# Kernel optimization log

Measured on AMD Instinct MI355X. Metric: run time of the kernel, lower is better.

The kernel has to match this reference:

```python
import jax, jax.numpy as jnp
import numpy as np

N_NODES = 50000
N_EDGES = 400000
N_GRAPHS = 256
HID = 128
FEAT_IN, POS_IN, EDGE_IN = 64, 16, 16
N_LAYERS = 4


def _lin(x, w, b):
    return x @ w.T + b


def setup_inputs() -> dict:
    key = jax.random.key(0)
    ks = iter(jax.random.split(key, 64))
    s = 0.05

    def w(shape):
        return (jax.random.normal(next(ks), shape, dtype=jnp.float32) * s)

    inp = {
        "h": jax.random.normal(next(ks), (N_NODES, FEAT_IN), dtype=jnp.float32),
        "e": jax.random.normal(next(ks), (N_EDGES, EDGE_IN), dtype=jnp.float32),
        "p": jax.random.normal(next(ks), (N_NODES, POS_IN), dtype=jnp.float32),
        "edge_index": jax.random.randint(next(ks), (2, N_EDGES), 0, N_NODES),
        "batch": jnp.sort(jax.random.randint(next(ks), (N_NODES,), 0, N_GRAPHS)),
        # embeddings
        "h_embed_w": w((HID, FEAT_IN)), "h_embed_b": w((HID,)),
        "e_embed_w": w((HID, EDGE_IN)), "e_embed_b": w((HID,)),
        "p_embed_w": w((HID, POS_IN)), "p_embed_b": w((HID,)),
        # per-layer params, stacked over layers
        "hu_w": w((N_LAYERS, HID, 5 * HID)), "hu_b": w((N_LAYERS, HID)),
        "eu_w": w((N_LAYERS, HID, 3 * HID)), "eu_b": w((N_LAYERS, HID)),
        "pu_w": w((N_LAYERS, HID, 3 * HID)), "pu_b": w((N_LAYERS, HID)),
        "hagg_w": w((N_LAYERS, HID, 2 * HID)), "hagg_b": w((N_LAYERS, HID)),
        "pagg_w": w((N_LAYERS, HID, 2 * HID)), "pagg_b": w((N_LAYERS, HID)),
        # readout MLP
        "r1_w": w((HID, 2 * HID)), "r1_b": w((HID,)),
        "r2_w": w((HID // 2, HID)), "r2_b": w((HID // 2,)),
        "r3_w": w((1, HID // 2)), "r3_b": w((1,)),
    }
    return inp


def reference(h, e, p, edge_index, batch,
              h_embed_w, h_embed_b, e_embed_w, e_embed_b, p_embed_w, p_embed_b,
              hu_w, hu_b, eu_w, eu_b, pu_w, pu_b,
              hagg_w, hagg_b, pagg_w, pagg_b,
              r1_w, r1_b, r2_w, r2_b, r3_w, r3_b):
    send, rec = edge_index[0], edge_index[1]
    N = h.shape[0]

    h = _lin(h, h_embed_w, h_embed_b)
    e = _lin(e, e_embed_w, e_embed_b)
    p = _lin(p, p_embed_w, p_embed_b)

    for l in range(N_LAYERS):
        hp_send = jnp.concatenate((h[send], p[send]), axis=1)  # [E, 2H]
        hp_rec = jnp.concatenate((h[rec], p[rec]), axis=1)     # [E, 2H]
        h_msg = _lin(jnp.concatenate((hp_send, hp_rec, e), axis=1), hu_w[l], hu_b[l])
        h_msg_agg = jax.ops.segment_sum(h_msg, rec, num_segments=N)
        h = _lin(jnp.concatenate((h, h_msg_agg), axis=1), hagg_w[l], hagg_b[l])
        e = _lin(jnp.concatenate((h[send], h[rec], e), axis=1), eu_w[l], eu_b[l])
        p_msg = _lin(jnp.concatenate((p[send], p[rec], e), axis=1), pu_w[l], pu_b[l])
        p_msg_agg = jax.ops.segment_sum(p_msg, rec, num_segments=N)
        p = _lin(jnp.concatenate((p, p_msg_agg), axis=1), pagg_w[l], pagg_b[l])

    h_agg = jax.ops.segment_sum(h, batch, num_segments=N_GRAPHS)
    p_agg = jax.ops.segment_sum(p, batch, num_segments=N_GRAPHS)
    hep = jnp.concatenate((h_agg, p_agg), axis=1)
    x = jax.nn.relu(_lin(hep, r1_w, r1_b))
    x = jax.nn.relu(_lin(x, r2_w, r2_b))
    out = _lin(x, r3_w, r3_b).squeeze(-1)  # [N_GRAPHS]
    return (out, p)
```

## Files before the change

kernel.cpp:

```cpp
#include <hip/hip_runtime.h>

typedef __attribute__((ext_vector_type(8))) short bf16x8;
typedef __attribute__((ext_vector_type(4))) float f32x4;
typedef __attribute__((ext_vector_type(4))) unsigned short us4;

__device__ __forceinline__ float b2f(unsigned short h) {
  union { unsigned int u; float f; } v; v.u = ((unsigned int)h) << 16; return v.f;
}
__device__ __forceinline__ unsigned short f2b(float f) {
  union { float f; unsigned int u; } v; v.f = f;
  unsigned int r = v.u + 0x7fffu + ((v.u >> 16) & 1u);
  return (unsigned short)(r >> 16);
}

__device__ __forceinline__ bf16x8 scale8(bf16x8 a, float d) {
  bf16x8 r;
#pragma unroll
  for (int i = 0; i < 8; ++i) {
    union { unsigned int u; float f; } v;
    v.u = ((unsigned int)(unsigned short)a[i]) << 16;
    v.f *= d;
    r[i] = (short)(v.u >> 16);
  }
  return r;
}

__global__ void f2b_kernel(const float* __restrict__ in, unsigned short* __restrict__ out, int n4) {
  int i = blockIdx.x * blockDim.x + threadIdx.x;
  int stride = gridDim.x * blockDim.x;
  for (; i < n4; i += stride) {
    float4 v = reinterpret_cast<const float4*>(in)[i];
    us4 o;
    o[0] = f2b(v.x); o[1] = f2b(v.y); o[2] = f2b(v.z); o[3] = f2b(v.w);
    reinterpret_cast<us4*>(out)[i] = o;
  }
}

__launch_bounds__(256)
__global__ void compose_w(const float* __restrict__ hg, const float* __restrict__ hu,
                          const float* __restrict__ pg, const float* __restrict__ pu,
                          const float* __restrict__ hub, const float* __restrict__ pub,
                          unsigned short* __restrict__ wh, unsigned short* __restrict__ wp,
                          float* __restrict__ bh, float* __restrict__ bp) {
  __shared__ float As[128][129];
  __shared__ float Bs[128][36];
  __shared__ float bvs[128];
  const int l = blockIdx.x >> 5, t = blockIdx.x & 31;
  const float* A; const float* B; const float* bv; unsigned short* W; float* bo;
  int lda, ldb, ldw, cbase, wbase, dbase;
  if (t < 20) {
    A = hg + (size_t)l * 128 * 256; lda = 256;
    B = hu + (size_t)l * 128 * 640; ldb = 640;
    W = wh + (size_t)l * 128 * 768; ldw = 768;
    bv = hub + l * 128; bo = bh + l * 128; cbase = t * 32;
    wbase = (cbase < 256) ? cbase : (cbase < 512 ? cbase + 256 : cbase - 256);
    dbase = 384;
  } else {
    A = pg + (size_t)l * 128 * 256; lda = 256;
    B = pu + (size_t)l * 128 * 384; ldb = 384;
    W = wp + (size_t)l * 128 * 512; ldw = 512;
    bv = pub + l * 128; bo = bp + l * 128; cbase = (t - 20) * 32;
    wbase = (cbase < 128) ? cbase : (cbase < 256 ? cbase + 256 : cbase - 128);
    dbase = 256;
  }
  const int tid = threadIdx.x;
  for (int idx = tid; idx < 128 * 128; idx += 256) {
    int r = idx >> 7, c = idx & 127;
    As[r][c] = A[r * lda + 128 + c];
  }
  for (int idx = tid; idx < 128 * 32; idx += 256) {
    int m = idx >> 5, c = idx & 31;
    Bs[m][c] = B[m * ldb + cbase + c];
  }
  if (tid < 128) bvs[tid] = bv[tid];
  __syncthreads();
  const int o = tid & 127, g = tid >> 7;
  float acc[16];
#pragma unroll
  for (int j = 0; j < 16; ++j) acc[j] = 0.f;
  for (int m = 0; m < 128; ++m) {
    float a = As[o][m];
#pragma unroll
    for (int j4 = 0; j4 < 4; ++j4) {
      float4 b4 = *reinterpret_cast<const float4*>(&Bs[m][g * 16 + j4 * 4]);
      acc[j4 * 4 + 0] += a * b4.x; acc[j4 * 4 + 1] += a * b4.y;
      acc[j4 * 4 + 2] += a * b4.z; acc[j4 * 4 + 3] += a * b4.w;
    }
  }
#pragma unroll
  for (int j4 = 0; j4 < 4; ++j4) {
    us4 ov;
    ov[0] = f2b(acc[j4 * 4 + 0]); ov[1] = f2b(acc[j4 * 4 + 1]);
    ov[2] = f2b(acc[j4 * 4 + 2]); ov[3] = f2b(acc[j4 * 4 + 3]);
    *reinterpret_cast<us4*>(&W[(long)o * ldw + wbase + g * 16 + j4 * 4]) = ov;
  }
  if (cbase == 0) {
    for (int idx = tid; idx < 128 * 128; idx += 256) {
      int oo = idx >> 7, m = idx & 127;
      W[(long)oo * ldw + dbase + m] = f2b(A[oo * lda + m]);
    }
    if (tid < 128) {
      float s = 0.f;
      for (int m = 0; m < 128; ++m) s += As[tid][m] * bvs[m];
      bo[tid] = s;
    }
  }
}

template<int K>
__launch_bounds__(256)
__global__ void embed_fast(const float* __restrict__ in, const float* __restrict__ w,
                           const float* __restrict__ b, unsigned short* __restrict__ out,
                           long M, int ostride, int ocoloff, const float* __restrict__ degB) {
  __shared__ float wT[K][129];
  __shared__ float xt[16 * K];
  const int tid = threadIdx.x;
  const int col = tid & 127;
  const int half = tid >> 7;
  for (int idx = tid; idx < 128 * K; idx += 256) {
    int c = idx / K, k = idx % K;
    wT[k][c] = w[idx];
  }
  __syncthreads();
  float wreg[K];
#pragma unroll
  for (int k = 0; k < K; ++k) wreg[k] = wT[k][col];
  const float bcol = b[col];

  for (long r0 = (long)blockIdx.x * 16; r0 < M; r0 += (long)gridDim.x * 16) {
    __syncthreads();
    const float4* src4 = reinterpret_cast<const float4*>(in + r0 * K);
    const int n4 = 16 * K / 4;
    if (r0 + 16 <= M) {
      for (int i = tid; i < n4; i += 256)
        reinterpret_cast<float4*>(xt)[i] = src4[i];
    } else {
      int rem = (int)((M - r0) * K) / 4;
      for (int i = tid; i < n4; i += 256) {
        float4 z = {0.f, 0.f, 0.f, 0.f};
        reinterpret_cast<float4*>(xt)[i] = (i < rem) ? src4[i] : z;
      }
    }
    __syncthreads();
#pragma unroll
    for (int rr = 0; rr < 8; ++rr) {
      long row = r0 + half * 8 + rr;
      if (row >= M) break;
      const float* xr = &xt[(half * 8 + rr) * K];
      float acc = bcol * (degB ? degB[row] : 1.0f);
#pragma unroll
      for (int k4 = 0; k4 < K / 4; ++k4) {
        float4 xv = reinterpret_cast<const float4*>(xr)[k4];
        acc += xv.x * wreg[k4 * 4] + xv.y * wreg[k4 * 4 + 1] +
               xv.z * wreg[k4 * 4 + 2] + xv.w * wreg[k4 * 4 + 3];
      }
      out[row * ostride + ocoloff + col] = f2b(acc);
    }
  }
}

__global__ void count_deg(const int* __restrict__ rec, int* __restrict__ deg, int E) {
  int i = blockIdx.x * blockDim.x + threadIdx.x;
  if (i < E) atomicAdd(&deg[rec[i]], 1);
}

__global__ void scan_blk(const int* __restrict__ deg, int* __restrict__ tmp,
                         int* __restrict__ blkSum, int N) {
  __shared__ int ts[256];
  const int b = blockIdx.x, t = threadIdx.x;
  const int base = b * 1024 + t * 4;
  int v0 = (base + 0 < N) ? deg[base + 0] : 0;
  int v1 = (base + 1 < N) ? deg[base + 1] : 0;
  int v2 = (base + 2 < N) ? deg[base + 2] : 0;
  int v3 = (base + 3 < N) ? deg[base + 3] : 0;
  int tsum = v0 + v1 + v2 + v3;
  ts[t] = tsum;
  __syncthreads();
  for (int off = 1; off < 256; off <<= 1) {
    int x = (t >= off) ? ts[t - off] : 0;
    __syncthreads();
    ts[t] += x;
    __syncthreads();
  }
  int texcl = ts[t] - tsum;
  if (base + 0 < N) tmp[base + 0] = texcl;
  if (base + 1 < N) tmp[base + 1] = texcl + v0;
  if (base + 2 < N) tmp[base + 2] = texcl + v0 + v1;
  if (base + 3 < N) tmp[base + 3] = texcl + v0 + v1 + v2;
  if (t == 255) blkSum[b] = ts[255];
}

__global__ void scan_top(int* __restrict__ blkSum, int nb) {
  __shared__ int s[64];
  int t = threadIdx.x;
  if (t < nb) s[t] = blkSum[t];
  __syncthreads();
  if (t == 0) {
    int run = 0;
    for (int i = 0; i < nb; ++i) { int x = s[i]; s[i] = run; run += x; }
  }
  __syncthreads();
  if (t < nb) blkSum[t] = s[t];
}

__global__ void scan_fix(const int* __restrict__ deg, int* __restrict__ row_ptr,
                         const int* __restrict__ blkOff, int* __restrict__ cursor,
                         float* __restrict__ degF, int N, int E) {
  const int b = blockIdx.x, t = threadIdx.x;
  const int base = b * 1024 + t * 4;
  const int off = blkOff[b];
#pragma unroll
  for (int k = 0; k < 4; ++k) {
    int i = base + k;
    if (i < N) {
      int v = row_ptr[i] + off;
      row_ptr[i] = v;
      cursor[i] = v;
      degF[i] = (float)deg[i];
    }
  }
  if (b == 0 && t == 0) row_ptr[N] = E;
}

__global__ void scatter_perm(const int* __restrict__ rec, const int* __restrict__ send,
                             int* __restrict__ cursor, int* __restrict__ perm,
                             int* __restrict__ sendP, int E) {
  int i = blockIdx.x * blockDim.x + threadIdx.x;
  if (i < E) {
    int pos = atomicAdd(&cursor[rec[i]], 1);
    perm[pos] = i;
    sendP[pos] = send[i];
  }
}

__global__ void segsum_raw(const float* __restrict__ eraw, const int* __restrict__ row_ptr,
                           const int* __restrict__ perm, float* __restrict__ out16, int N) {
  int sub = threadIdx.x >> 4;
  int f = threadIdx.x & 15;
  int r = blockIdx.x * 16 + sub;
  if (r >= N) return;
  int j0 = row_ptr[r], j1 = row_ptr[r + 1];
  float s0 = 0.f, s1 = 0.f;
  int j = j0;
  for (; j + 2 <= j1; j += 2) {
    int e0 = perm[j], e1 = perm[j + 1];
    s0 += eraw[(long)e0 * 16 + f];
    s1 += eraw[(long)e1 * 16 + f];
  }
  if (j < j1) s0 += eraw[(long)perm[j] * 16 + f];
  out16[(long)r * 16 + f] = s0 + s1;
}

__launch_bounds__(256)
__global__ void gather_sum256(const unsigned short* __restrict__ src,
                              const int* __restrict__ row_ptr, const int* __restrict__ sendP,
                              unsigned short* __restrict__ dst, int N) {
  const int wid = threadIdx.x >> 6, lane = threadIdx.x & 63;
  const int r = blockIdx.x * 4 + wid;
  if (r >= N) return;
  const int j0 = row_ptr[r], j1 = row_ptr[r + 1];
  const int off = lane * 4;
  float a0 = 0.f, a1 = 0.f, a2 = 0.f, a3 = 0.f;
  int j = j0;
  for (; j + 4 <= j1; j += 4) {
    int i0 = sendP[j], i1 = sendP[j + 1], i2 = sendP[j + 2], i3 = sendP[j + 3];
    us4 x = *reinterpret_cast<const us4*>(&src[(long)i0 * 256 + off]);
    us4 y = *reinterpret_cast<const us4*>(&src[(long)i1 * 256 + off]);
    us4 z = *reinterpret_cast<const us4*>(&src[(long)i2 * 256 + off]);
    us4 w = *reinterpret_cast<const us4*>(&src[(long)i3 * 256 + off]);
    a0 += b2f(x[0]) + b2f(y[0]) + b2f(z[0]) + b2f(w[0]);
    a1 += b2f(x[1]) + b2f(y[1]) + b2f(z[1]) + b2f(w[1]);
    a2 += b2f(x[2]) + b2f(y[2]) + b2f(z[2]) + b2f(w[2]);
    a3 += b2f(x[3]) + b2f(y[3]) + b2f(z[3]) + b2f(w[3]);
  }
  for (; j < j1; ++j) {
    us4 x = *reinterpret_cast<const us4*>(&src[(long)sendP[j] * 256 + off]);
    a0 += b2f(x[0]); a1 += b2f(x[1]); a2 += b2f(x[2]); a3 += b2f(x[3]);
  }
  us4 o;
  o[0] = f2b(a0); o[1] = f2b(a1); o[2] = f2b(a2); o[3] = f2b(a3);
  *reinterpret_cast<us4*>(&dst[(long)r * 256 + off]) = o;
}

__launch_bounds__(256)
__global__ void gather_sum128(const unsigned short* __restrict__ src, int col,
                              const int* __restrict__ row_ptr, const int* __restrict__ sendP,
                              unsigned short* __restrict__ dst, int N) {
  const int wid = threadIdx.x >> 6, lane = threadIdx.x & 63;
  const int r = blockIdx.x * 4 + wid;
  if (r >= N) return;
  const int j0 = row_ptr[r], j1 = row_ptr[r + 1];
  const int half = lane >> 5;
  const int c = lane & 31;
  const int off = col + c * 4;
  float a0 = 0.f, a1 = 0.f, a2 = 0.f, a3 = 0.f;
  float b0 = 0.f, b1 = 0.f, b2 = 0.f, b3 = 0.f;
  int j = j0 + half;
  for (; j + 6 < j1; j += 8) {
    int i0 = sendP[j], i1 = sendP[j + 2], i2 = sendP[j + 4], i3 = sendP[j + 6];
    us4 x = *reinterpret_cast<const us4*>(&src[(long)i0 * 256 + off]);
    us4 y = *reinterpret_cast<const us4*>(&src[(long)i1 * 256 + off]);
    us4 z = *reinterpret_cast<const us4*>(&src[(long)i2 * 256 + off]);
    us4 w = *reinterpret_cast<const us4*>(&src[(long)i3 * 256 + off]);
    a0 += b2f(x[0]) + b2f(z[0]); a1 += b2f(x[1]) + b2f(z[1]);
    a2 += b2f(x[2]) + b2f(z[2]); a3 += b2f(x[3]) + b2f(z[3]);
    b0 += b2f(y[0]) + b2f(w[0]); b1 += b2f(y[1]) + b2f(w[1]);
    b2 += b2f(y[2]) + b2f(w[2]); b3 += b2f(y[3]) + b2f(w[3]);
  }
  for (; j + 2 < j1; j += 4) {
    int i0 = sendP[j], i1 = sendP[j + 2];
    us4 x = *reinterpret_cast<const us4*>(&src[(long)i0 * 256 + off]);
    us4 y = *reinterpret_cast<const us4*>(&src[(long)i1 * 256 + off]);
    a0 += b2f(x[0]); a1 += b2f(x[1]); a2 += b2f(x[2]); a3 += b2f(x[3]);
    b0 += b2f(y[0]); b1 += b2f(y[1]); b2 += b2f(y[2]); b3 += b2f(y[3]);
  }
  if (j < j1) {
    us4 x = *reinterpret_cast<const us4*>(&src[(long)sendP[j] * 256 + off]);
    a0 += b2f(x[0]); a1 += b2f(x[1]); a2 += b2f(x[2]); a3 += b2f(x[3]);
  }
  a0 += b0; a1 += b1; a2 += b2; a3 += b3;
  a0 += __shfl_xor(a0, 32); a1 += __shfl_xor(a1, 32);
  a2 += __shfl_xor(a2, 32); a3 += __shfl_xor(a3, 32);
  if (half == 0) {
    us4 o;
    o[0] = f2b(a0); o[1] = f2b(a1); o[2] = f2b(a2); o[3] = f2b(a3);
    *reinterpret_cast<us4*>(&dst[(long)r * 256 + off]) = o;
  }
}

__launch_bounds__(256, 3)
__global__ void gemm_mp(int M, int nsrc, int Kw, int srcsel, int coloffs, int sflags,
                        const unsigned short* __restrict__ sp0, const unsigned short* __restrict__ sp1,
                        const unsigned short* __restrict__ sp2,
                        const unsigned short* __restrict__ Wb,
                        const float* __restrict__ bdeg, const float* __restrict__ bone,
                        const float* __restrict__ degF,
                        unsigned short* __restrict__ outB, int ostride, int ocoloff,
                        float* __restrict__ outF) {
  __shared__ __align__(16) unsigned short ldsW[8 * 64 * 8];
  const int tid = threadIdx.x;
  const int wid = tid >> 6, lane = tid & 63;
  const long rowBase = (long)blockIdx.x * 128 + wid * 32;
  const int lq = lane >> 4;
  const int lr = lane & 15;

  int rowD[2];
  float degD[2];
#pragma unroll
  for (int am = 0; am < 2; ++am) {
    long e = rowBase + am * 16 + lr;
    if (e >= M) e = M - 1;
    rowD[am] = (int)e;
    degD[am] = degF[rowD[am]];
  }

  f32x4 acc[2][8];
#pragma unroll
  for (int i = 0; i < 2; ++i)
#pragma unroll
    for (int j = 0; j < 8; ++j) acc[i][j] = 0.f;

  int wcol = 0;
  for (int si = 0; si < nsrc; ++si) {
    const int sel = (srcsel >> (si * 4)) & 15;
    const unsigned short* sp = (sel == 0) ? sp0 : (sel == 1) ? sp1 : sp2;
    const long astride = (sel == 2) ? 128 : 256;
    const int acoloff = ((coloffs >> (si * 4)) & 15) * 128;
    const int f = (sflags >> (si * 4)) & 15;
    const int nrep = (f == 1) ? 2 : 1;
#pragma unroll 4
    for (int sub = 0; sub < 4; ++sub) {
      const int koff = acoloff + sub * 32 + lq * 8;
      bf16x8 a[2];
#pragma unroll
      for (int am = 0; am < 2; ++am)
        a[am] = *reinterpret_cast<const bf16x8*>(&sp[(long)rowD[am] * astride + koff]);
      for (int rep = 0; rep < nrep; ++rep) {
        const bool sc = (f == 2) || (rep == 1);
        const int wk = wcol + rep * 128 + sub * 32;
        __syncthreads();
#pragma unroll
        for (int it = 0; it < 2; ++it) {
          int idx = tid + it * 256;
          int t = idx >> 6, l = idx & 63;
          int n = t * 16 + (l & 15);
          int kk = wk + ((l >> 4) * 8);
          *reinterpret_cast<bf16x8*>(&ldsW[idx * 8]) =
              *reinterpret_cast<const bf16x8*>(&Wb[(long)n * Kw + kk]);
        }
        __syncthreads();
        bf16x8 av0 = sc ? scale8(a[0], degD[0]) : a[0];
        bf16x8 av1 = sc ? scale8(a[1], degD[1]) : a[1];
#pragma unroll
        for (int n = 0; n < 8; ++n) {
          bf16x8 b = *reinterpret_cast<const bf16x8*>(&ldsW[(n * 64 + lane) * 8]);
          acc[0][n] = __builtin_amdgcn_mfma_f32_16x16x32_bf16(av0, b, acc[0][n], 0, 0, 0);
          acc[1][n] = __builtin_amdgcn_mfma_f32_16x16x32_bf16(av1, b, acc[1][n], 0, 0, 0);
        }
      }
    }
    wcol += nrep * 128;
  }

  float bd[8], bo[8];
#pragma unroll
  for (int n = 0; n < 8; ++n) {
    bd[n] = bdeg ? bdeg[n * 16 + lr] : 0.f;
    bo[n] = bone ? bone[n * 16 + lr] : 0.f;
  }

#pragma unroll
  for (int am = 0; am < 2; ++am) {
#pragma unroll
    for (int r = 0; r < 4; ++r) {
      long row = rowBase + am * 16 + lq * 4 + r;
      if (row < M) {
        float d = degF[row];
        long ob = row * ostride + ocoloff;
#pragma unroll
        for (int n = 0; n < 8; ++n) {
          float v = acc[am][n][r] + bd[n] * d + bo[n];
          outB[ob + n * 16 + lr] = f2b(v);
          if (outF) outF[row * 128 + n * 16 + lr] = v;
        }
      }
    }
  }
}

__global__ void readout_agg(const unsigned short* __restrict__ hp,
                            const int* __restrict__ batch, float* __restrict__ hep, int N) {
  int col = threadIdx.x;
  int n0 = blockIdx.x * 128;
  int n1 = n0 + 128; if (n1 > N) n1 = N;
  float sum = 0.f; int curg = -1;
  for (int n = n0; n < n1; ++n) {
    int g = batch[n];
    if (g != curg) {
      if (curg >= 0) unsafeAtomicAdd(&hep[(long)curg * 256 + col], sum);
      curg = g; sum = 0.f;
    }
    sum += b2f(hp[(long)n * 256 + col]);
  }
  if (curg >= 0) unsafeAtomicAdd(&hep[(long)curg * 256 + col], sum);
}

__global__ void mlp_kernel(const float* __restrict__ hep,
                           const float* __restrict__ r1w, const float* __restrict__ r1b,
                           const float* __restrict__ r2w, const float* __restrict__ r2b,
                           const float* __restrict__ r3w, const float* __restrict__ r3b,
                           float* __restrict__ out) {
  int g = blockIdx.x, t = threadIdx.x;
  __shared__ float x[256];
  __shared__ float y[128];
  __shared__ float z[64];
  x[t] = hep[(long)g * 256 + t];
  x[t + 128] = hep[(long)g * 256 + 128 + t];
  __syncthreads();
  float s = r1b[t];
  for (int k = 0; k < 256; ++k) s += r1w[t * 256 + k] * x[k];
  y[t] = fmaxf(s, 0.f);
  __syncthreads();
  if (t < 64) {
    float s2 = r2b[t];
    for (int k = 0; k < 128; ++k) s2 += r2w[t * 128 + k] * y[k];
    z[t] = fmaxf(s2, 0.f);
  }
  __syncthreads();
  if (t == 0) {
    float s3 = r3b[0];
    for (int k = 0; k < 64; ++k) s3 += r3w[k] * z[k];
    out[g] = s3;
  }
}

extern "C" void kernel_launch(void* const* d_in, const int* in_sizes, int n_in,
                              void* d_out, int out_size, void* d_ws, size_t ws_size,
                              hipStream_t stream) {
  const float* h_in = (const float*)d_in[0];
  const float* e_in = (const float*)d_in[1];
  const float* p_in = (const float*)d_in[2];
  const int* ei = (const int*)d_in[3];
  const int* batch = (const int*)d_in[4];
  const float* he_w = (const float*)d_in[5];  const float* he_b = (const float*)d_in[6];
  const float* ee_w = (const float*)d_in[7];  const float* ee_b = (const float*)d_in[8];
  const float* pe_w = (const float*)d_in[9];  const float* pe_b = (const float*)d_in[10];
  const float* hu_w = (const float*)d_in[11]; const float* hu_b = (const float*)d_in[12];
  const float* eu_w = (const float*)d_in[13]; const float* eu_b = (const float*)d_in[14];
  const float* pu_w = (const float*)d_in[15]; const float* pu_b = (const float*)d_in[16];
  const float* hg_w = (const float*)d_in[17]; const float* hg_b = (const float*)d_in[18];
  const float* pg_w = (const float*)d_in[19]; const float* pg_b = (const float*)d_in[20];
  const float* r1w = (const float*)d_in[21];  const float* r1b = (const float*)d_in[22];
  const float* r2w = (const float*)d_in[23];  const float* r2b = (const float*)d_in[24];
  const float* r3w = (const float*)d_in[25];  const float* r3b = (const float*)d_in[26];

  const int N = 50000, E = 400000, G = 256;
  const int* send = ei;
  const int* rec = ei + E;

  char* ws = (char*)d_ws;
  size_t off = 0;
  auto alloc = [&](size_t bytes) {
    void* pp = ws + off;
    off += (bytes + 255) & ~(size_t)255;
    return pp;
  };
  unsigned short* hp  = (unsigned short*)alloc((size_t)N * 256 * 2);
  unsigned short* gHP = (unsigned short*)alloc((size_t)N * 256 * 2);
  unsigned short* sT  = (unsigned short*)alloc((size_t)N * 128 * 2);
  float* segsumF = (float*)alloc((size_t)N * 16 * 4);
  int* deg = (int*)alloc((size_t)N * 4);
  int* row_ptr = (int*)alloc((size_t)(N + 1) * 4);
  int* cursor = (int*)alloc((size_t)N * 4);
  int* blkSum = (int*)alloc((size_t)64 * 4);
  int* perm = (int*)alloc((size_t)E * 4);
  int* sendP = (int*)alloc((size_t)E * 4);
  float* degF = (float*)alloc((size_t)N * 4);
  float* hep = (float*)alloc((size_t)G * 256 * 4);
  unsigned short* w_h2 = (unsigned short*)alloc((size_t)4 * 128 * 768 * 2);
  unsigned short* w_p2 = (unsigned short*)alloc((size_t)4 * 128 * 512 * 2);
  unsigned short* w_eu = (unsigned short*)alloc((size_t)4 * 128 * 384 * 2);
  float* bh1 = (float*)alloc((size_t)4 * 128 * 4);
  float* bp1 = (float*)alloc((size_t)4 * 128 * 4);
  (void)ws_size; (void)n_in; (void)in_sizes; (void)out_size;

  f2b_kernel<<<192, 256, 0, stream>>>(eu_w, w_eu, 4 * 128 * 384 / 4);
  compose_w<<<128, 256, 0, stream>>>(hg_w, hu_w, pg_w, pu_w, hu_b, pu_b, w_h2, w_p2, bh1, bp1);

  const int nb = (N + 1023) / 1024;
  hipMemsetAsync(deg, 0, (size_t)N * 4, stream);
  count_deg<<<(E + 255) / 256, 256, 0, stream>>>(rec, deg, E);
  scan_blk<<<nb, 256, 0, stream>>>(deg, row_ptr, blkSum, N);
  scan_top<<<1, 64, 0, stream>>>(blkSum, nb);
  scan_fix<<<nb, 256, 0, stream>>>(deg, row_ptr, blkSum, cursor, degF, N, E);
  scatter_perm<<<(E + 255) / 256, 256, 0, stream>>>(rec, send, cursor, perm, sendP, E);

  embed_fast<64><<<3125, 256, 0, stream>>>(h_in, he_w, he_b, hp, N, 256, 0, nullptr);
  embed_fast<16><<<3125, 256, 0, stream>>>(p_in, pe_w, pe_b, hp, N, 256, 128, nullptr);
  segsum_raw<<<(N + 15) / 16, 256, 0, stream>>>(e_in, row_ptr, perm, segsumF, N);
  embed_fast<16><<<3125, 256, 0, stream>>>(segsumF, ee_w, ee_b, sT, N, 128, 0, degF);

  gather_sum256<<<(N + 3) / 4, 256, 0, stream>>>(hp, row_ptr, sendP, gHP, N);

  float* pOut = (float*)d_out + 256;
  const int gridN = (N + 127) / 128;
  const int gridG = (N + 3) / 4;

  for (int l = 0; l < 4; ++l) {
    gemm_mp<<<gridN, 256, 0, stream>>>(N, 5, 768, 0x11200, 0x10010, 0x21000,
        gHP, hp, sT,
        w_h2 + (size_t)l * 128 * 768, bh1 + l * 128, hg_b + l * 128, degF,
        hp, 256, 0, nullptr);
    gather_sum128<<<gridG, 256, 0, stream>>>(hp, 0, row_ptr, sendP, gHP, N);
    gemm_mp<<<gridN, 256, 0, stream>>>(N, 3, 384, 0x210, 0x000, 0x020,
        gHP, hp, sT,
        w_eu + (size_t)l * 128 * 384, eu_b + l * 128, nullptr, degF,
        sT, 128, 0, nullptr);
    gemm_mp<<<gridN, 256, 0, stream>>>(N, 3, 512, 0x120, 0x101, 0x100,
        gHP, hp, sT,
        w_p2 + (size_t)l * 128 * 512, bp1 + l * 128, pg_b + l * 128, degF,
        hp, 256, 128, (l == 3) ? pOut : nullptr);
    if (l < 3)
      gather_sum128<<<gridG, 256, 0, stream>>>(hp, 128, row_ptr, sendP, gHP, N);
  }

  hipMemsetAsync(hep, 0, (size_t)G * 256 * 4, stream);
  readout_agg<<<(N + 127) / 128, 256, 0, stream>>>(hp, batch, hep, N);
  mlp_kernel<<<G, 128, 0, stream>>>(hep, r1w, r1b, r2w, r2b, r3w, r3b, (float*)d_out);
}
```

Measured before the change: 658.7 us.

## Stage 64-wide K tiles in gemm_mp and run h-embedding on MFMA

gemm_mp now loads two 32-wide K slices of the weight into a doubled LDS buffer per sync pair, which halves the number of __syncthreads barriers in the main loop. The input h embedding, previously an FP32 scalar kernel, becomes a bf16 MFMA kernel fed by new conversion kernels for h_in and its weight. scale8 now rounds to nearest instead of truncating. The changes add extra conversion launches and more LDS per block, which could lower occupancy, and they lower the precision of the embedding.

```diff
diff --git a/kernel.cpp b/kernel.cpp
--- a/kernel.cpp
+++ b/kernel.cpp
@@ -19,8 +19,7 @@
   for (int i = 0; i < 8; ++i) {
     union { unsigned int u; float f; } v;
     v.u = ((unsigned int)(unsigned short)a[i]) << 16;
-    v.f *= d;
-    r[i] = (short)(v.u >> 16);
+    r[i] = (short)f2b(v.f * d);
   }
   return r;
 }
@@ -107,6 +106,74 @@
   }
 }
 
+__launch_bounds__(256, 3)
+__global__ void embed_mfma64(const unsigned short* __restrict__ xb, const unsigned short* __restrict__ w64,
+                             const float* __restrict__ b, unsigned short* __restrict__ out, int M) {
+  __shared__ __align__(16) unsigned short ldsW[2 * 8 * 64 * 8];
+  const int tid = threadIdx.x;
+  const int wid = tid >> 6, lane = tid & 63;
+  const long rowBase = (long)blockIdx.x * 128 + wid * 32;
+  const int lq = lane >> 4;
+  const int lr = lane & 15;
+
+#pragma unroll
+  for (int it = 0; it < 4; ++it) {
+    int f = tid + it * 256;
+    int sub = f >> 9, r = f & 511;
+    int t = r >> 6, l = r & 63;
+    int n = t * 16 + (l & 15);
+    int kk = sub * 32 + ((l >> 4) * 8);
+    *reinterpret_cast<bf16x8*>(&ldsW[f * 8]) =
+        *reinterpret_cast<const bf16x8*>(&w64[(long)n * 64 + kk]);
+  }
+  __syncthreads();
+
+  int rowD[2];
+#pragma unroll
+  for (int am = 0; am < 2; ++am) {
+    long e = rowBase + am * 16 + lr;
+    if (e >= M) e = M - 1;
+    rowD[am] = (int)e;
+  }
+
+  f32x4 acc[2][8];
+#pragma unroll
+  for (int i = 0; i < 2; ++i)
+#pragma unroll
+    for (int j = 0; j < 8; ++j) acc[i][j] = 0.f;
+
+#pragma unroll
+  for (int s = 0; s < 2; ++s) {
+    bf16x8 a[2];
+#pragma unroll
+    for (int am = 0; am < 2; ++am)
+      a[am] = *reinterpret_cast<const bf16x8*>(&xb[(long)rowD[am] * 64 + s * 32 + lq * 8]);
+#pragma unroll
+    for (int n = 0; n < 8; ++n) {
+      bf16x8 bb = *reinterpret_cast<const bf16x8*>(&ldsW[((s << 9) + (n << 6) + lane) * 8]);
+      acc[0][n] = __builtin_amdgcn_mfma_f32_16x16x32_bf16(a[0], bb, acc[0][n], 0, 0, 0);
+      acc[1][n] = __builtin_amdgcn_mfma_f32_16x16x32_bf16(a[1], bb, acc[1][n], 0, 0, 0);
+    }
+  }
+
+  float bo[8];
+#pragma unroll
+  for (int n = 0; n < 8; ++n) bo[n] = b[n * 16 + lr];
+
+#pragma unroll
+  for (int am = 0; am < 2; ++am) {
+#pragma unroll
+    for (int r = 0; r < 4; ++r) {
+      long row = rowBase + am * 16 + lq * 4 + r;
+      if (row < M) {
+#pragma unroll
+        for (int n = 0; n < 8; ++n)
+          out[row * 256 + n * 16 + lr] = f2b(acc[am][n][r] + bo[n]);
+      }
+    }
+  }
+}
+
 template<int K>
 __launch_bounds__(256)
 __global__ void embed_fast(const float* __restrict__ in, const float* __restrict__ w,
@@ -337,7 +404,7 @@
                         const float* __restrict__ degF,
                         unsigned short* __restrict__ outB, int ostride, int ocoloff,
                         float* __restrict__ outF) {
-  __shared__ __align__(16) unsigned short ldsW[8 * 64 * 8];
+  __shared__ __align__(16) unsigned short ldsW[2 * 8 * 64 * 8];
   const int tid = threadIdx.x;
   const int wid = tid >> 6, lane = tid & 63;
   const long rowBase = (long)blockIdx.x * 128 + wid * 32;
@@ -368,34 +435,41 @@
     const int acoloff = ((coloffs >> (si * 4)) & 15) * 128;
     const int f = (sflags >> (si * 4)) & 15;
     const int nrep = (f == 1) ? 2 : 1;
-#pragma unroll 4
-    for (int sub = 0; sub < 4; ++sub) {
-      const int koff = acoloff + sub * 32 + lq * 8;
-      bf16x8 a[2];
-#pragma unroll
-      for (int am = 0; am < 2; ++am)
-        a[am] = *reinterpret_cast<const bf16x8*>(&sp[(long)rowD[am] * astride + koff]);
-      for (int rep = 0; rep < nrep; ++rep) {
-        const bool sc = (f == 2) || (rep == 1);
-        const int wk = wcol + rep * 128 + sub * 32;
+    for (int rep = 0; rep < nrep; ++rep) {
+      const bool sc = (f == 2) || (rep == 1);
+      const int wbase = wcol + rep * 128;
+#pragma unroll 2
+      for (int h = 0; h < 2; ++h) {
+        bf16x8 a[2][2];
+#pragma unroll
+        for (int s = 0; s < 2; ++s) {
+          const int koff = acoloff + h * 64 + s * 32 + lq * 8;
+#pragma unroll
+          for (int am = 0; am < 2; ++am)
+            a[am][s] = *reinterpret_cast<const bf16x8*>(&sp[(long)rowD[am] * astride + koff]);
+        }
         __syncthreads();
 #pragma unroll
-        for (int it = 0; it < 2; ++it) {
-          int idx = tid + it * 256;
-          int t = idx >> 6, l = idx & 63;
+        for (int it = 0; it < 4; ++it) {
+          int fi = tid + it * 256;
+          int sub = fi >> 9, r = fi & 511;
+          int t = r >> 6, l = r & 63;
           int n = t * 16 + (l & 15);
-          int kk = wk + ((l >> 4) * 8);
-          *reinterpret_cast<bf16x8*>(&ldsW[idx * 8]) =
+          int kk = wbase + h * 64 + sub * 32 + ((l >> 4) * 8);
+          *reinterpret_cast<bf16x8*>(&ldsW[fi * 8]) =
               *reinterpret_cast<const bf16x8*>(&Wb[(long)n * Kw + kk]);
         }
         __syncthreads();
-        bf16x8 av0 = sc ? scale8(a[0], degD[0]) : a[0];
-        bf16x8 av1 = sc ? scale8(a[1], degD[1]) : a[1];
-#pragma unroll
-        for (int n = 0; n < 8; ++n) {
-          bf16x8 b = *reinterpret_cast<const bf16x8*>(&ldsW[(n * 64 + lane) * 8]);
-          acc[0][n] = __builtin_amdgcn_mfma_f32_16x16x32_bf16(av0, b, acc[0][n], 0, 0, 0);
-          acc[1][n] = __builtin_amdgcn_mfma_f32_16x16x32_bf16(av1, b, acc[1][n], 0, 0, 0);
+#pragma unroll
+        for (int s = 0; s < 2; ++s) {
+          bf16x8 av0 = sc ? scale8(a[0][s], degD[0]) : a[0][s];
+          bf16x8 av1 = sc ? scale8(a[1][s], degD[1]) : a[1][s];
+#pragma unroll
+          for (int n = 0; n < 8; ++n) {
+            bf16x8 b = *reinterpret_cast<const bf16x8*>(&ldsW[((s << 9) + (n << 6) + lane) * 8]);
+            acc[0][n] = __builtin_amdgcn_mfma_f32_16x16x32_bf16(av0, b, acc[0][n], 0, 0, 0);
+            acc[1][n] = __builtin_amdgcn_mfma_f32_16x16x32_bf16(av1, b, acc[1][n], 0, 0, 0);
+          }
         }
       }
     }
@@ -508,6 +582,8 @@
   unsigned short* hp  = (unsigned short*)alloc((size_t)N * 256 * 2);
   unsigned short* gHP = (unsigned short*)alloc((size_t)N * 256 * 2);
   unsigned short* sT  = (unsigned short*)alloc((size_t)N * 128 * 2);
+  unsigned short* hb16 = (unsigned short*)alloc((size_t)N * 64 * 2);
+  unsigned short* w_he = (unsigned short*)alloc((size_t)128 * 64 * 2);
   float* segsumF = (float*)alloc((size_t)N * 16 * 4);
   int* deg = (int*)alloc((size_t)N * 4);
   int* row_ptr = (int*)alloc((size_t)(N + 1) * 4);
@@ -525,6 +601,8 @@
   (void)ws_size; (void)n_in; (void)in_sizes; (void)out_size;
 
   f2b_kernel<<<192, 256, 0, stream>>>(eu_w, w_eu, 4 * 128 * 384 / 4);
+  f2b_kernel<<<2048, 256, 0, stream>>>(h_in, hb16, N * 64 / 4);
+  f2b_kernel<<<8, 256, 0, stream>>>(he_w, w_he, 128 * 64 / 4);
   compose_w<<<128, 256, 0, stream>>>(hg_w, hu_w, pg_w, pu_w, hu_b, pu_b, w_h2, w_p2, bh1, bp1);
 
   const int nb = (N + 1023) / 1024;
@@ -535,7 +613,7 @@
   scan_fix<<<nb, 256, 0, stream>>>(deg, row_ptr, blkSum, cursor, degF, N, E);
   scatter_perm<<<(E + 255) / 256, 256, 0, stream>>>(rec, send, cursor, perm, sendP, E);
 
-  embed_fast<64><<<3125, 256, 0, stream>>>(h_in, he_w, he_b, hp, N, 256, 0, nullptr);
+  embed_mfma64<<<(N + 127) / 128, 256, 0, stream>>>(hb16, w_he, he_b, hp, N);
   embed_fast<16><<<3125, 256, 0, stream>>>(p_in, pe_w, pe_b, hp, N, 256, 128, nullptr);
   segsum_raw<<<(N + 15) / 16, 256, 0, stream>>>(e_in, row_ptr, perm, segsumF, N);
   embed_fast<16><<<3125, 256, 0, stream>>>(segsumF, ee_w, ee_b, sT, N, 128, 0, degF);
```

Result: slower. 733.8 us (+11.4%).
